# Kernel tuning notes

Hardware: AMD Instinct MI355X
Metric: run time of the kernel (lower is better)

Reference implementation:

```python
import jax, jax.numpy as jnp
import numpy as np

NEUMANN_TERMS = 6  # matches neumann_terms=6 in init_kwargs


def cayley_apply(W, x, terms):
    """Apply Cayley-parameterized unitary U = (I - A)^{-1}(I + A), A = skew(W),
    with the inverse approximated by a truncated Neumann series:
    (I - A)^{-1} z ~= sum_{k=0}^{terms-1} A^k z.  x: [N, d] row vectors."""
    A = 0.5 * (W - W.T)            # skew-symmetric [d, d]
    z = x + x @ A.T                # (I + A) x
    acc = z
    s = z
    for _ in range(terms - 1):     # small fixed loop over Neumann terms
        s = s @ A.T                # A^k z
        acc = acc + s
    return acc


def quantum_activation(h, theta):
    """Parametric quantum rotation: rotate each adjacent feature pair by theta.
    Norm-preserving (unitary) nonlinearity in place of ReLU/GELU."""
    a = h[..., 0::2]
    b = h[..., 1::2]
    c = jnp.cos(theta)
    s = jnp.sin(theta)
    ra = a * c - b * s
    rb = a * s + b * c
    return jnp.stack([ra, rb], axis=-1).reshape(h.shape)


def setup_inputs() -> dict:
    key = jax.random.key(0)
    k1, k2, k3 = jax.random.split(key, 3)
    num_tokens, d_model = 16384, 2048
    x = jax.random.normal(k1, (num_tokens, d_model), dtype=jnp.float32)
    # Orthogonal(gain=0.1)-like init: small-norm weights keep the Neumann series convergent
    u1 = 0.1 * jax.random.normal(k2, (d_model, d_model), dtype=jnp.float32) / jnp.sqrt(d_model)
    u1 = u1 * jnp.sqrt(d_model) * 0.0 + 0.1 * jax.random.orthogonal(k2, d_model, dtype=jnp.float32)
    u2 = 0.1 * jax.random.orthogonal(k3, d_model, dtype=jnp.float32)
    theta = jnp.asarray(0.7854, dtype=jnp.float32)  # pi/4 initializer
    return {"x": x, "u1": u1, "u2": u2, "theta": theta}


def reference(x, u1, u2, theta):
    h = cayley_apply(u1, x, NEUMANN_TERMS)
    h = quantum_activation(h, theta)
    out = cayley_apply(u2, h, NEUMANN_TERMS)
    return out
```

## Files before the change

### kernel.cpp

```cpp
#include <hip/hip_runtime.h>
#include <hip/hip_bf16.h>

#define ND 2048

using bf16 = __hip_bfloat16;
using short8 = __attribute__((ext_vector_type(8))) short;
using floatx4 = __attribute__((ext_vector_type(4))) float;

__device__ __forceinline__ void gl2lds16(const short* g, short* l) {
    __builtin_amdgcn_global_load_lds(
        (const __attribute__((address_space(1))) unsigned int*)g,
        (__attribute__((address_space(3))) unsigned int*)l,
        16, 0, 0);
}


__global__ void build_skew(const float* __restrict__ u, bf16* __restrict__ M) {
    __shared__ float t[32][33];
    const int bx = blockIdx.x & (ND / 32 - 1);
    const int by = blockIdx.x / (ND / 32);
    const int tx = threadIdx.x & 31;
    const int ty = threadIdx.x >> 5;
#pragma unroll
    for (int rr = 0; rr < 4; ++rr) {
        const int r = ty * 4 + rr;
        t[tx][r] = u[(size_t)(bx * 32 + r) * ND + by * 32 + tx];
    }
    __syncthreads();
#pragma unroll
    for (int rr = 0; rr < 4; ++rr) {
        const int r = ty * 4 + rr;
        const size_t idx = (size_t)(by * 32 + r) * ND + bx * 32 + tx;
        M[idx] = __float2bfloat16(0.5f * (t[r][tx] - u[idx]));
    }
}

__global__ void build_hoff1(const bf16* __restrict__ M, const bf16* Msq, bf16* Hoff) {
    const size_t idx = (size_t)blockIdx.x * 256 + threadIdx.x;
    const float m = __bfloat162float(M[idx]);
    const float q = __bfloat162float(Msq[idx]);
    Hoff[idx] = __float2bfloat16(2.f * m + q);
}

__global__ void build_hoff(const bf16* M, const bf16* Msq, bf16* Hoff, bf16* HoffT) {
    const size_t idx = (size_t)blockIdx.x * 256 + threadIdx.x;
    const float m = __bfloat162float(M[idx]);
    const float q = __bfloat162float(Msq[idx]);
    Hoff[idx] = __float2bfloat16(2.f * m + q);
    HoffT[idx] = __float2bfloat16(q - 2.f * m);
}

__global__ void convert_f32_bf16(const float* __restrict__ x, bf16* __restrict__ y) {
    const size_t base = ((size_t)blockIdx.x * 256 + threadIdx.x) * 8;
    const float4 f0 = *(const float4*)(x + base);
    const float4 f1 = *(const float4*)(x + base + 4);
    short8 pk;
    pk[0] = __builtin_bit_cast(short, __float2bfloat16(f0.x));
    pk[1] = __builtin_bit_cast(short, __float2bfloat16(f0.y));
    pk[2] = __builtin_bit_cast(short, __float2bfloat16(f0.z));
    pk[3] = __builtin_bit_cast(short, __float2bfloat16(f0.w));
    pk[4] = __builtin_bit_cast(short, __float2bfloat16(f1.x));
    pk[5] = __builtin_bit_cast(short, __float2bfloat16(f1.y));
    pk[6] = __builtin_bit_cast(short, __float2bfloat16(f1.z));
    pk[7] = __builtin_bit_cast(short, __float2bfloat16(f1.w));
    *(short8*)((short*)y + base) = pk;
}

enum { EPI_PLAIN = 0, EPI_NEG = 1, EPI_ADD1 = 2, EPI_P = 3, EPI_P_ROT = 4, EPI_PT = 5 };

template <int EPI, bool OF32>
__device__ __forceinline__ void gemm_core(
    short* aT, short* bT,
    const bf16* __restrict__ A, const bf16* __restrict__ Bt, void* __restrict__ Cp,
    const int Nc, const int K, const int bx, const int by,
    const bf16* __restrict__ add1, const bf16* __restrict__ add2,
    const float* __restrict__ thetaP)
{
    const int tid = threadIdx.x;
    const int lane = tid & 63;
    const int quad = lane >> 4;
    const int l15 = lane & 15;
    const int wv = tid >> 6;
    const int wr = (wv >> 1) << 6;
    const int wc = (wv & 1) << 6;

    const short* Ag = (const short*)A + (size_t)(by << 7) * K;
    const short* Bg = (const short*)Bt + (size_t)(bx << 7) * K;

    floatx4 acc[4][4];
#pragma unroll
    for (int i = 0; i < 4; ++i)
#pragma unroll
        for (int j = 0; j < 4; ++j)
            acc[i][j] = (floatx4){0.f, 0.f, 0.f, 0.f};

    for (int k0 = 0; k0 < K; k0 += 32) {
#pragma unroll
        for (int c = 0; c < 2; ++c) {
            const int ch = (c << 8) + (wv << 6) + lane;
            const int row = ch >> 2;
            const int kp = (ch & 3) << 3;
            const int ldsBase = ((c << 8) + (wv << 6)) << 3;
            gl2lds16(Ag + (size_t)row * K + k0 + kp, aT + ldsBase);
            gl2lds16(Bg + (size_t)row * K + k0 + kp, bT + ldsBase);
        }
        __syncthreads();
        short8 af[4], bfr[4];
#pragma unroll
        for (int mi = 0; mi < 4; ++mi)
            af[mi] = *(const short8*)(aT + ((wr + (mi << 4) + l15) << 5) + (quad << 3));
#pragma unroll
        for (int ni = 0; ni < 4; ++ni)
            bfr[ni] = *(const short8*)(bT + ((wc + (ni << 4) + l15) << 5) + (quad << 3));
#pragma unroll
        for (int mi = 0; mi < 4; ++mi)
#pragma unroll
            for (int ni = 0; ni < 4; ++ni)
                acc[mi][ni] = __builtin_amdgcn_mfma_f32_16x16x32_bf16(af[mi], bfr[ni], acc[mi][ni], 0, 0, 0);
        __syncthreads();
    }

    float ct = 0.f, st = 0.f;
    if (EPI == EPI_P_ROT) {
        const float th = *thetaP;
        ct = cosf(th);
        st = sinf(th);
    }

#pragma unroll
    for (int mi = 0; mi < 4; ++mi) {
#pragma unroll
        for (int ni = 0; ni < 4; ++ni) {
#pragma unroll
            for (int r = 0; r < 4; ++r) {
                const int row = (by << 7) + wr + (mi << 4) + (quad << 2) + r;
                const int col = (bx << 7) + wc + (ni << 4) + l15;
                const size_t idx = (size_t)row * Nc + col;
                float v = acc[mi][ni][r];
                if (EPI == EPI_NEG) v = -v;
                if (EPI == EPI_ADD1) v += __bfloat162float(add1[idx]);
                if (EPI == EPI_P)
                    v += (row == col ? 1.f : 0.f)
                       + __bfloat162float(add1[idx]) + __bfloat162float(add2[idx]);
                if (EPI == EPI_PT)
                    v += (row == col ? 1.f : 0.f)
                       + __bfloat162float(add1[idx])
                       + __bfloat162float(add2[(size_t)col * Nc + row]);
                if (EPI == EPI_P_ROT) {
                    v += (row == col ? 1.f : 0.f)
                       + __bfloat162float(add1[idx]) + __bfloat162float(add2[idx]);
                    const float w = __shfl_xor(v, 1, 64);
                    v = (l15 & 1) ? (st * w + ct * v) : (ct * v - st * w);
                }
                if (OF32) ((float*)Cp)[idx] = v;
                else      ((bf16*)Cp)[idx] = __float2bfloat16(v);
            }
        }
    }
}

template <int EPI, bool OF32>
__launch_bounds__(256, 2) __global__
void gemm_one(const bf16* __restrict__ A, const bf16* __restrict__ Bt,
              void* __restrict__ Cp, const int Nc, const int K,
              const bf16* __restrict__ add1, const bf16* __restrict__ add2,
              const float* __restrict__ thetaP)
{
    __shared__ __attribute__((aligned(16))) short aT[128 * 32];
    __shared__ __attribute__((aligned(16))) short bT[128 * 32];
    const int nblk = Nc >> 7;
    gemm_core<EPI, OF32>(aT, bT, A, Bt, Cp, Nc, K, blockIdx.x % nblk, blockIdx.x / nblk,
                         add1, add2, thetaP);
}

template <int EPI0, int EPI1>
__launch_bounds__(256, 2) __global__
void gemm_dual(const bf16* A0, const bf16* B0, bf16* C0, const bf16* a10, const bf16* a20,
               const bf16* A1, const bf16* B1, bf16* C1, const bf16* a11, const bf16* a21,
               const float* thetaP)
{
    __shared__ __attribute__((aligned(16))) short aT[128 * 32];
    __shared__ __attribute__((aligned(16))) short bT[128 * 32];
    const int nblk = ND >> 7;
    const int nsub = nblk * nblk;
    int b = blockIdx.x;
    if (b < nsub) {
        gemm_core<EPI0, false>(aT, bT, A0, B0, (void*)C0, ND, ND, b % nblk, b / nblk, a10, a20, thetaP);
    } else {
        b -= nsub;
        gemm_core<EPI1, false>(aT, bT, A1, B1, (void*)C1, ND, ND, b % nblk, b / nblk, a11, a21, thetaP);
    }
}


__device__ __forceinline__ void stage512(short* ldsT, const short* gT, const int K,
                                         const int kb, const int c0,
                                         const int wv, const int lane) {
    const int ch = c0 + (wv << 6) + lane;
    const int rw = ch >> 3;
    const int cs = (ch & 7) ^ (rw & 7);
    gl2lds16(gT + (size_t)rw * K + kb + (cs << 3),
             ldsT + ((c0 + (wv << 6)) << 3));
}

__device__ __forceinline__ void phase_mid() {
    __builtin_amdgcn_sched_barrier(0);
    __builtin_amdgcn_s_barrier();
    asm volatile("s_waitcnt lgkmcnt(0)" ::: "memory");
    __builtin_amdgcn_sched_barrier(0);
    __builtin_amdgcn_s_setprio(1);
}
__device__ __forceinline__ void phase_end() {
    __builtin_amdgcn_s_setprio(0);
    __builtin_amdgcn_sched_barrier(0);
    __builtin_amdgcn_s_barrier();
}

__device__ __forceinline__ void tile256(
    short* Ac, short* Bc, short* An,
    const short* Ag, const short* Bg, const int K, const int nt, const int t,
    const int wv, const int lane, const int aBase, const int bBase,
    const int cOff0, const int cOff1, floatx4 (&acc)[8][4])
{
    short8 af[4][2], bb[4][2];
    const int kb1 = (t + 1) << 6;
    const int kb2 = (t + 2) << 6;

#pragma unroll
    for (int ml = 0; ml < 4; ++ml) {
        af[ml][0] = *(const short8*)(Ac + aBase + (ml << 10) + cOff0);
        af[ml][1] = *(const short8*)(Ac + aBase + (ml << 10) + cOff1);
    }
#pragma unroll
    for (int ni = 0; ni < 2; ++ni) {
        bb[ni][0] = *(const short8*)(Bc + bBase + (ni << 10) + cOff0);
        bb[ni][1] = *(const short8*)(Bc + bBase + (ni << 10) + cOff1);
    }
    if (t + 1 < nt) { stage512(An, Ag, K, kb1, 512, wv, lane); stage512(An, Ag, K, kb1, 1536, wv, lane); }
    phase_mid();
#pragma unroll
    for (int ml = 0; ml < 4; ++ml)
#pragma unroll
        for (int ni = 0; ni < 2; ++ni) {
            acc[ml][ni] = __builtin_amdgcn_mfma_f32_16x16x32_bf16(af[ml][0], bb[ni][0], acc[ml][ni], 0, 0, 0);
            acc[ml][ni] = __builtin_amdgcn_mfma_f32_16x16x32_bf16(af[ml][1], bb[ni][1], acc[ml][ni], 0, 0, 0);
        }
    phase_end();

#pragma unroll
    for (int ni = 2; ni < 4; ++ni) {
        bb[ni][0] = *(const short8*)(Bc + bBase + (ni << 10) + cOff0);
        bb[ni][1] = *(const short8*)(Bc + bBase + (ni << 10) + cOff1);
    }
    if (t + 2 < nt) { stage512(Ac, Ag, K, kb2, 0, wv, lane); stage512(Ac, Ag, K, kb2, 1024, wv, lane); }
    phase_mid();
#pragma unroll
    for (int ml = 0; ml < 4; ++ml)
#pragma unroll
        for (int ni = 2; ni < 4; ++ni) {
            acc[ml][ni] = __builtin_amdgcn_mfma_f32_16x16x32_bf16(af[ml][0], bb[ni][0], acc[ml][ni], 0, 0, 0);
            acc[ml][ni] = __builtin_amdgcn_mfma_f32_16x16x32_bf16(af[ml][1], bb[ni][1], acc[ml][ni], 0, 0, 0);
        }
    phase_end();

#pragma unroll
    for (int ml = 0; ml < 4; ++ml) {
        af[ml][0] = *(const short8*)(Ac + aBase + 4096 + (ml << 10) + cOff0);
        af[ml][1] = *(const short8*)(Ac + aBase + 4096 + (ml << 10) + cOff1);
    }
    if (t + 2 < nt) { stage512(Bc, Bg, K, kb2, 0, wv, lane); stage512(Bc, Bg, K, kb2, 512, wv, lane); }
    phase_mid();
#pragma unroll
    for (int ml = 0; ml < 4; ++ml)
#pragma unroll
        for (int ni = 0; ni < 2; ++ni) {
            acc[4 + ml][ni] = __builtin_amdgcn_mfma_f32_16x16x32_bf16(af[ml][0], bb[ni][0], acc[4 + ml][ni], 0, 0, 0);
            acc[4 + ml][ni] = __builtin_amdgcn_mfma_f32_16x16x32_bf16(af[ml][1], bb[ni][1], acc[4 + ml][ni], 0, 0, 0);
        }
    phase_end();

    if (t + 2 < nt) { stage512(Bc, Bg, K, kb2, 1024, wv, lane); stage512(Bc, Bg, K, kb2, 1536, wv, lane); }
    __builtin_amdgcn_sched_barrier(0);
    if (t < nt - 2) asm volatile("s_waitcnt vmcnt(6)" ::: "memory");
    else            asm volatile("s_waitcnt vmcnt(0)" ::: "memory");
    __builtin_amdgcn_s_barrier();
    __builtin_amdgcn_sched_barrier(0);
    __builtin_amdgcn_s_setprio(1);
#pragma unroll
    for (int ml = 0; ml < 4; ++ml)
#pragma unroll
        for (int ni = 2; ni < 4; ++ni) {
            acc[4 + ml][ni] = __builtin_amdgcn_mfma_f32_16x16x32_bf16(af[ml][0], bb[ni][0], acc[4 + ml][ni], 0, 0, 0);
            acc[4 + ml][ni] = __builtin_amdgcn_mfma_f32_16x16x32_bf16(af[ml][1], bb[ni][1], acc[4 + ml][ni], 0, 0, 0);
        }
    phase_end();
}

__launch_bounds__(512, 2) __global__
void gemm_big256(const bf16* __restrict__ A, const bf16* __restrict__ Bt,
                 float* __restrict__ C, const int Nc, const int K)
{
    __shared__ __attribute__((aligned(16))) short smem[65536];
    short* A0s = smem;
    short* A1s = smem + 16384;
    short* B0s = smem + 32768;
    short* B1s = smem + 49152;

    const int nblkx = Nc >> 8;
    const int bx = blockIdx.x % nblkx;
    const int by = blockIdx.x / nblkx;
    const int tid = threadIdx.x;
    const int lane = tid & 63;
    const int q = lane >> 4;
    const int l15 = lane & 15;
    const int wv = tid >> 6;
    const int wm = wv >> 2;
    const int wn = wv & 3;

    const short* Ag = (const short*)A + (size_t)(by << 8) * K;
    const short* Bg = (const short*)Bt + (size_t)(bx << 8) * K;

    const int swz = l15 & 7;
    const int aBase = ((wm << 7) + l15) << 6;
    const int bBase = ((wn << 6) + l15) << 6;
    const int cOff0 = (q ^ swz) << 3;
    const int cOff1 = ((q + 4) ^ swz) << 3;

    floatx4 acc[8][4];
#pragma unroll
    for (int i = 0; i < 8; ++i)
#pragma unroll
        for (int j = 0; j < 4; ++j)
            acc[i][j] = (floatx4){0.f, 0.f, 0.f, 0.f};

    const int nt = K >> 6;

    stage512(A0s, Ag, K, 0, 0,    wv, lane);
    stage512(A0s, Ag, K, 0, 512,  wv, lane);
    stage512(A0s, Ag, K, 0, 1024, wv, lane);
    stage512(A0s, Ag, K, 0, 1536, wv, lane);
    stage512(B0s, Bg, K, 0, 0,    wv, lane);
    stage512(B0s, Bg, K, 0, 512,  wv, lane);
    stage512(B0s, Bg, K, 0, 1024, wv, lane);
    stage512(B0s, Bg, K, 0, 1536, wv, lane);
    stage512(A1s, Ag, K, 64, 0,    wv, lane);
    stage512(A1s, Ag, K, 64, 1024, wv, lane);
    stage512(B1s, Bg, K, 64, 0,    wv, lane);
    stage512(B1s, Bg, K, 64, 512,  wv, lane);
    stage512(B1s, Bg, K, 64, 1024, wv, lane);
    stage512(B1s, Bg, K, 64, 1536, wv, lane);
    __builtin_amdgcn_sched_barrier(0);
    asm volatile("s_waitcnt vmcnt(6)" ::: "memory");
    __builtin_amdgcn_s_barrier();

    for (int t = 0; t < nt; t += 2) {
        tile256(A0s, B0s, A1s, Ag, Bg, K, nt, t,     wv, lane, aBase, bBase, cOff0, cOff1, acc);
        tile256(A1s, B1s, A0s, Ag, Bg, K, nt, t + 1, wv, lane, aBase, bBase, cOff0, cOff1, acc);
    }

#pragma unroll
    for (int mi = 0; mi < 8; ++mi)
#pragma unroll
        for (int ni = 0; ni < 4; ++ni)
#pragma unroll
            for (int r = 0; r < 4; ++r) {
                const int row = (by << 8) + (wm << 7) + (mi << 4) + (q << 2) + r;
                const int col = (bx << 8) + (wn << 6) + (ni << 4) + l15;
                C[(size_t)row * Nc + col] = acc[mi][ni][r];
            }
}

template <int EPI, bool AF32, bool OF32>
__launch_bounds__(256, 2) __global__
void gemm_bt(const void* __restrict__ Ap, const bf16* __restrict__ Bt,
             void* __restrict__ Cp, const int Nc, const int K,
             const bf16* __restrict__ add1, const bf16* __restrict__ add2,
             const float* __restrict__ thetaP)
{
    __shared__ __attribute__((aligned(16))) short aT[128 * 32];
    __shared__ __attribute__((aligned(16))) short bT[128 * 32];

    const int nblk = Nc >> 7;
    const int bx = blockIdx.x % nblk;
    const int by = blockIdx.x / nblk;
    const int tid = threadIdx.x;
    const int lane = tid & 63;
    const int quad = lane >> 4;
    const int l15 = lane & 15;
    const int wv = tid >> 6;
    const int wr = (wv >> 1) << 6;
    const int wc = (wv & 1) << 6;

    const short* Ag = (const short*)Ap + (size_t)(by << 7) * K;
    const float* Agf = (const float*)Ap + (size_t)(by << 7) * K;
    const short* Bg = (const short*)Bt + (size_t)(bx << 7) * K;

    floatx4 acc[4][4];
#pragma unroll
    for (int i = 0; i < 4; ++i)
#pragma unroll
        for (int j = 0; j < 4; ++j)
            acc[i][j] = (floatx4){0.f, 0.f, 0.f, 0.f};

    for (int k0 = 0; k0 < K; k0 += 32) {
#pragma unroll
        for (int c = 0; c < 2; ++c) {
            const int ch = tid + (c << 8);
            const int row = ch >> 2;
            const int kp = (ch & 3) << 3;
            if (AF32) {
                const float4 f0 = *(const float4*)(Agf + (size_t)row * K + k0 + kp);
                const float4 f1 = *(const float4*)(Agf + (size_t)row * K + k0 + kp + 4);
                short8 pk;
                pk[0] = __builtin_bit_cast(short, __float2bfloat16(f0.x));
                pk[1] = __builtin_bit_cast(short, __float2bfloat16(f0.y));
                pk[2] = __builtin_bit_cast(short, __float2bfloat16(f0.z));
                pk[3] = __builtin_bit_cast(short, __float2bfloat16(f0.w));
                pk[4] = __builtin_bit_cast(short, __float2bfloat16(f1.x));
                pk[5] = __builtin_bit_cast(short, __float2bfloat16(f1.y));
                pk[6] = __builtin_bit_cast(short, __float2bfloat16(f1.z));
                pk[7] = __builtin_bit_cast(short, __float2bfloat16(f1.w));
                *(short8*)(aT + (row << 5) + kp) = pk;
            } else {
                *(int4*)(aT + (row << 5) + kp) = *(const int4*)(Ag + (size_t)row * K + k0 + kp);
            }
            *(int4*)(bT + (row << 5) + kp) = *(const int4*)(Bg + (size_t)row * K + k0 + kp);
        }
        __syncthreads();
        short8 af[4], bfr[4];
#pragma unroll
        for (int mi = 0; mi < 4; ++mi)
            af[mi] = *(const short8*)(aT + ((wr + (mi << 4) + l15) << 5) + (quad << 3));
#pragma unroll
        for (int ni = 0; ni < 4; ++ni)
            bfr[ni] = *(const short8*)(bT + ((wc + (ni << 4) + l15) << 5) + (quad << 3));
#pragma unroll
        for (int mi = 0; mi < 4; ++mi)
#pragma unroll
            for (int ni = 0; ni < 4; ++ni)
                acc[mi][ni] = __builtin_amdgcn_mfma_f32_16x16x32_bf16(af[mi], bfr[ni], acc[mi][ni], 0, 0, 0);
        __syncthreads();
    }

    float ct = 0.f, st = 0.f;
    if (EPI == EPI_P_ROT) {
        const float th = *thetaP;
        ct = cosf(th);
        st = sinf(th);
    }

#pragma unroll
    for (int mi = 0; mi < 4; ++mi) {
#pragma unroll
        for (int ni = 0; ni < 4; ++ni) {
#pragma unroll
            for (int r = 0; r < 4; ++r) {
                const int row = (by << 7) + wr + (mi << 4) + (quad << 2) + r;
                const int col = (bx << 7) + wc + (ni << 4) + l15;
                const size_t idx = (size_t)row * Nc + col;
                float v = acc[mi][ni][r];
                if (EPI == EPI_NEG) v = -v;
                if (EPI == EPI_ADD1) v += __bfloat162float(add1[idx]);
                if (EPI == EPI_P || EPI == EPI_P_ROT)
                    v += (row == col ? 1.f : 0.f)
                       + __bfloat162float(add1[idx]) + __bfloat162float(add2[idx]);
                if (EPI == EPI_P_ROT) {
                    const float w = __shfl_xor(v, 1, 64);
                    v = (l15 & 1) ? (st * w + ct * v) : (ct * v - st * w);
                }
                if (OF32) ((float*)Cp)[idx] = v;
                else      ((bf16*)Cp)[idx] = __float2bfloat16(v);
            }
        }
    }
}


extern "C" void kernel_launch(void* const* d_in, const int* in_sizes, int n_in,
                              void* d_out, int out_size, void* d_ws, size_t ws_size,
                              hipStream_t stream)
{
    const float* x = (const float*)d_in[0];
    const float* u1 = (const float*)d_in[1];
    const float* u2 = (const float*)d_in[2];
    const float* th = (const float*)d_in[3];
    float* out = (float*)d_out;
    const int tokens = in_sizes[0] / ND;

    const size_t MAT = (size_t)ND * ND;
    const size_t XBE = (size_t)tokens * ND;

    const dim3 blk(256);
    const int gSkew = (ND / 32) * (ND / 32);
    const int gElem = (int)(MAT / 256);
    const int gSm = (ND / 128) * (ND / 128);
    const int gBig = (tokens / 128) * (ND / 128);

    if (ws_size >= (6 * MAT + XBE) * sizeof(bf16)) {
        bf16* base = (bf16*)d_ws;
        bf16* b0 = base;
        bf16* b1 = base + MAT;
        bf16* b2 = base + 2 * MAT;
        bf16* b3 = base + 3 * MAT;
        bf16* b4 = base + 4 * MAT;
        bf16* b5 = base + 5 * MAT;
        bf16* xb = base + 6 * MAT;

        convert_f32_bf16<<<(int)(XBE / 2048), blk, 0, stream>>>(x, xb);
        build_skew<<<gSkew, blk, 0, stream>>>(u2, b0);
        build_skew<<<gSkew, blk, 0, stream>>>(u1, b1);
        gemm_dual<EPI_NEG, EPI_NEG><<<2 * gSm, blk, 0, stream>>>(
            b0, b0, b2, nullptr, nullptr,  b1, b1, b3, nullptr, nullptr, nullptr);
        gemm_dual<EPI_ADD1, EPI_ADD1><<<2 * gSm, blk, 0, stream>>>(
            b2, b2, b4, b2, nullptr,  b3, b3, b5, b3, nullptr, nullptr);
        build_hoff1<<<gElem, blk, 0, stream>>>(b0, b2, b2);
        build_hoff1<<<gElem, blk, 0, stream>>>(b1, b3, b3);
        gemm_dual<EPI_PT, EPI_P_ROT><<<2 * gSm, blk, 0, stream>>>(
            b4, b2, b0, b4, b2,  b3, b5, b1, b5, b3, th);
        gemm_one<EPI_PLAIN, false><<<gSm, blk, 0, stream>>>(b0, b1, b2, ND, ND, nullptr, nullptr, nullptr);
        if ((tokens & 255) == 0) {
            const int gBig256 = (tokens >> 8) * (ND >> 8);
            gemm_big256<<<gBig256, dim3(512), 0, stream>>>(xb, b2, out, ND, ND);
        } else {
            gemm_one<EPI_PLAIN, true><<<gBig, blk, 0, stream>>>(xb, b2, out, ND, ND, nullptr, nullptr, nullptr);
        }
    } else {
        bf16* A = (bf16*)d_ws;
        bf16* B = A + MAT;
        bf16* Cb = B + MAT;
        bf16* D = Cb + MAT;
        bf16* E = D + MAT;

        build_skew<<<gSkew, blk, 0, stream>>>(u2, A);
        gemm_bt<EPI_NEG, false, false><<<gSm, blk, 0, stream>>>(A, A, B, ND, ND, nullptr, nullptr, nullptr);
        gemm_bt<EPI_ADD1, false, false><<<gSm, blk, 0, stream>>>(B, B, Cb, ND, ND, B, nullptr, nullptr);
        build_hoff<<<gElem, blk, 0, stream>>>(A, B, D, E);
        gemm_bt<EPI_P, false, false><<<gSm, blk, 0, stream>>>(Cb, D, A, ND, ND, Cb, E, nullptr);

        build_skew<<<gSkew, blk, 0, stream>>>(u1, B);
        gemm_bt<EPI_NEG, false, false><<<gSm, blk, 0, stream>>>(B, B, Cb, ND, ND, nullptr, nullptr, nullptr);
        gemm_bt<EPI_ADD1, false, false><<<gSm, blk, 0, stream>>>(Cb, Cb, D, ND, ND, Cb, nullptr, nullptr);
        build_hoff<<<gElem, blk, 0, stream>>>(B, Cb, E, B);
        gemm_bt<EPI_P_ROT, false, false><<<gSm, blk, 0, stream>>>(E, D, Cb, ND, ND, D, E, th);

        gemm_bt<EPI_PLAIN, false, false><<<gSm, blk, 0, stream>>>(A, Cb, D, ND, ND, nullptr, nullptr, nullptr);
        gemm_bt<EPI_PLAIN, true, true><<<gBig, blk, 0, stream>>>(x, D, out, ND, ND, nullptr, nullptr, nullptr);
    }
}
```

Before: 598.6 us.

## Software-pipeline LDS fragment loads across phases and add XCD-aware block swizzle

Restructures the 256x256 GEMM main loop so that A/B register fragments for the next phase and next k-tile are read from LDS one phase ahead, with partial lgkmcnt waits instead of full drains. The aim is to overlap LDS reads with MFMA work instead of stalling on them. It also remaps block indices so consecutive tiles land on the same XCD, improving L2 reuse across all GEMM kernels. This raises register pressure and depends on hand-tuned vmcnt/lgkmcnt counts, which are easy to get wrong.

```diff
diff --git a/kernel.cpp b/kernel.cpp
--- a/kernel.cpp
+++ b/kernel.cpp
@@ -12,6 +12,11 @@
         (const __attribute__((address_space(1))) unsigned int*)g,
         (__attribute__((address_space(3))) unsigned int*)l,
         16, 0, 0);
+}
+
+__device__ __forceinline__ int xcd_swz(int b, int g) {
+    if ((g & 7) == 0) b = (b & 7) * (g >> 3) + (b >> 3);
+    return b;
 }
 
 
@@ -169,7 +174,8 @@
     __shared__ __attribute__((aligned(16))) short aT[128 * 32];
     __shared__ __attribute__((aligned(16))) short bT[128 * 32];
     const int nblk = Nc >> 7;
-    gemm_core<EPI, OF32>(aT, bT, A, Bt, Cp, Nc, K, blockIdx.x % nblk, blockIdx.x / nblk,
+    const int b = xcd_swz(blockIdx.x, gridDim.x);
+    gemm_core<EPI, OF32>(aT, bT, A, Bt, Cp, Nc, K, b % nblk, b / nblk,
                          add1, add2, thetaP);
 }
 
@@ -183,7 +189,7 @@
     __shared__ __attribute__((aligned(16))) short bT[128 * 32];
     const int nblk = ND >> 7;
     const int nsub = nblk * nblk;
-    int b = blockIdx.x;
+    int b = xcd_swz(blockIdx.x, gridDim.x);
     if (b < nsub) {
         gemm_core<EPI0, false>(aT, bT, A0, B0, (void*)C0, ND, ND, b % nblk, b / nblk, a10, a20, thetaP);
     } else {
@@ -203,86 +209,104 @@
              ldsT + ((c0 + (wv << 6)) << 3));
 }
 
-__device__ __forceinline__ void phase_mid() {
-    __builtin_amdgcn_sched_barrier(0);
-    __builtin_amdgcn_s_barrier();
-    asm volatile("s_waitcnt lgkmcnt(0)" ::: "memory");
-    __builtin_amdgcn_sched_barrier(0);
-    __builtin_amdgcn_s_setprio(1);
-}
 __device__ __forceinline__ void phase_end() {
     __builtin_amdgcn_s_setprio(0);
     __builtin_amdgcn_sched_barrier(0);
     __builtin_amdgcn_s_barrier();
 }
 
-__device__ __forceinline__ void tile256(
-    short* Ac, short* Bc, short* An,
+#define MFMA_BF16 __builtin_amdgcn_mfma_f32_16x16x32_bf16
+
+__device__ __forceinline__ void tile256p(
+    short* Ac, short* Bc, short* An, short* Bn,
     const short* Ag, const short* Bg, const int K, const int nt, const int t,
     const int wv, const int lane, const int aBase, const int bBase,
-    const int cOff0, const int cOff1, floatx4 (&acc)[8][4])
-{
-    short8 af[4][2], bb[4][2];
+    const int cOff0, const int cOff1,
+    short8 (&afLo)[4][2], short8 (&afHi)[4][2], short8 (&bb)[4][2],
+    floatx4 (&acc)[8][4])
+{
     const int kb1 = (t + 1) << 6;
     const int kb2 = (t + 2) << 6;
-
-#pragma unroll
-    for (int ml = 0; ml < 4; ++ml) {
-        af[ml][0] = *(const short8*)(Ac + aBase + (ml << 10) + cOff0);
-        af[ml][1] = *(const short8*)(Ac + aBase + (ml << 10) + cOff1);
-    }
-#pragma unroll
-    for (int ni = 0; ni < 2; ++ni) {
-        bb[ni][0] = *(const short8*)(Bc + bBase + (ni << 10) + cOff0);
-        bb[ni][1] = *(const short8*)(Bc + bBase + (ni << 10) + cOff1);
-    }
-    if (t + 1 < nt) { stage512(An, Ag, K, kb1, 512, wv, lane); stage512(An, Ag, K, kb1, 1536, wv, lane); }
-    phase_mid();
-#pragma unroll
-    for (int ml = 0; ml < 4; ++ml)
-#pragma unroll
-        for (int ni = 0; ni < 2; ++ni) {
-            acc[ml][ni] = __builtin_amdgcn_mfma_f32_16x16x32_bf16(af[ml][0], bb[ni][0], acc[ml][ni], 0, 0, 0);
-            acc[ml][ni] = __builtin_amdgcn_mfma_f32_16x16x32_bf16(af[ml][1], bb[ni][1], acc[ml][ni], 0, 0, 0);
-        }
-    phase_end();
+    const bool sfull = (t < nt - 2);
 
 #pragma unroll
     for (int ni = 2; ni < 4; ++ni) {
         bb[ni][0] = *(const short8*)(Bc + bBase + (ni << 10) + cOff0);
         bb[ni][1] = *(const short8*)(Bc + bBase + (ni << 10) + cOff1);
     }
+#pragma unroll
+    for (int ml = 0; ml < 4; ++ml) {
+        afHi[ml][0] = *(const short8*)(Ac + aBase + 4096 + (ml << 10) + cOff0);
+        afHi[ml][1] = *(const short8*)(Ac + aBase + 4096 + (ml << 10) + cOff1);
+    }
+    if (t + 1 < nt) { stage512(An, Ag, K, kb1, 512, wv, lane); stage512(An, Ag, K, kb1, 1536, wv, lane); }
+    __builtin_amdgcn_sched_barrier(0);
+    __builtin_amdgcn_s_barrier();
+    asm volatile("s_waitcnt lgkmcnt(12)" ::: "memory");
+    __builtin_amdgcn_sched_barrier(0);
+    __builtin_amdgcn_s_setprio(1);
+#pragma unroll
+    for (int ml = 0; ml < 4; ++ml)
+#pragma unroll
+        for (int ni = 0; ni < 2; ++ni) {
+            acc[ml][ni] = MFMA_BF16(afLo[ml][0], bb[ni][0], acc[ml][ni], 0, 0, 0);
+            acc[ml][ni] = MFMA_BF16(afLo[ml][1], bb[ni][1], acc[ml][ni], 0, 0, 0);
+        }
+    phase_end();
+
     if (t + 2 < nt) { stage512(Ac, Ag, K, kb2, 0, wv, lane); stage512(Ac, Ag, K, kb2, 1024, wv, lane); }
-    phase_mid();
+    __builtin_amdgcn_sched_barrier(0);
+    if (sfull) asm volatile("s_waitcnt vmcnt(8)" ::: "memory");
+    else       asm volatile("s_waitcnt vmcnt(0)" ::: "memory");
+    __builtin_amdgcn_s_barrier();
+    asm volatile("s_waitcnt lgkmcnt(8)" ::: "memory");
+    __builtin_amdgcn_sched_barrier(0);
+    __builtin_amdgcn_s_setprio(1);
 #pragma unroll
     for (int ml = 0; ml < 4; ++ml)
 #pragma unroll
         for (int ni = 2; ni < 4; ++ni) {
-            acc[ml][ni] = __builtin_amdgcn_mfma_f32_16x16x32_bf16(af[ml][0], bb[ni][0], acc[ml][ni], 0, 0, 0);
-            acc[ml][ni] = __builtin_amdgcn_mfma_f32_16x16x32_bf16(af[ml][1], bb[ni][1], acc[ml][ni], 0, 0, 0);
+            acc[ml][ni] = MFMA_BF16(afLo[ml][0], bb[ni][0], acc[ml][ni], 0, 0, 0);
+            acc[ml][ni] = MFMA_BF16(afLo[ml][1], bb[ni][1], acc[ml][ni], 0, 0, 0);
         }
     phase_end();
 
-#pragma unroll
-    for (int ml = 0; ml < 4; ++ml) {
-        af[ml][0] = *(const short8*)(Ac + aBase + 4096 + (ml << 10) + cOff0);
-        af[ml][1] = *(const short8*)(Ac + aBase + 4096 + (ml << 10) + cOff1);
+    if (t + 1 < nt) {
+#pragma unroll
+        for (int ml = 0; ml < 4; ++ml) {
+            afLo[ml][0] = *(const short8*)(An + aBase + (ml << 10) + cOff0);
+            afLo[ml][1] = *(const short8*)(An + aBase + (ml << 10) + cOff1);
+        }
     }
     if (t + 2 < nt) { stage512(Bc, Bg, K, kb2, 0, wv, lane); stage512(Bc, Bg, K, kb2, 512, wv, lane); }
-    phase_mid();
+    __builtin_amdgcn_sched_barrier(0);
+    if (sfull) asm volatile("s_waitcnt vmcnt(6)" ::: "memory");
+    else       asm volatile("s_waitcnt vmcnt(0)" ::: "memory");
+    __builtin_amdgcn_s_barrier();
+    if (t + 1 < nt) asm volatile("s_waitcnt lgkmcnt(8)" ::: "memory");
+    else            asm volatile("s_waitcnt lgkmcnt(0)" ::: "memory");
+    __builtin_amdgcn_sched_barrier(0);
+    __builtin_amdgcn_s_setprio(1);
 #pragma unroll
     for (int ml = 0; ml < 4; ++ml)
 #pragma unroll
         for (int ni = 0; ni < 2; ++ni) {
-            acc[4 + ml][ni] = __builtin_amdgcn_mfma_f32_16x16x32_bf16(af[ml][0], bb[ni][0], acc[4 + ml][ni], 0, 0, 0);
-            acc[4 + ml][ni] = __builtin_amdgcn_mfma_f32_16x16x32_bf16(af[ml][1], bb[ni][1], acc[4 + ml][ni], 0, 0, 0);
+            acc[4 + ml][ni] = MFMA_BF16(afHi[ml][0], bb[ni][0], acc[4 + ml][ni], 0, 0, 0);
+            acc[4 + ml][ni] = MFMA_BF16(afHi[ml][1], bb[ni][1], acc[4 + ml][ni], 0, 0, 0);
         }
     phase_end();
 
+    if (t + 1 < nt) {
+#pragma unroll
+        for (int ni = 0; ni < 2; ++ni) {
+            bb[ni][0] = *(const short8*)(Bn + bBase + (ni << 10) + cOff0);
+            bb[ni][1] = *(const short8*)(Bn + bBase + (ni << 10) + cOff1);
+        }
+    }
     if (t + 2 < nt) { stage512(Bc, Bg, K, kb2, 1024, wv, lane); stage512(Bc, Bg, K, kb2, 1536, wv, lane); }
     __builtin_amdgcn_sched_barrier(0);
-    if (t < nt - 2) asm volatile("s_waitcnt vmcnt(6)" ::: "memory");
-    else            asm volatile("s_waitcnt vmcnt(0)" ::: "memory");
+    if (sfull) asm volatile("s_waitcnt vmcnt(6)" ::: "memory");
+    else       asm volatile("s_waitcnt vmcnt(0)" ::: "memory");
     __builtin_amdgcn_s_barrier();
     __builtin_amdgcn_sched_barrier(0);
     __builtin_amdgcn_s_setprio(1);
@@ -290,8 +314,8 @@
     for (int ml = 0; ml < 4; ++ml)
 #pragma unroll
         for (int ni = 2; ni < 4; ++ni) {
-            acc[4 + ml][ni] = __builtin_amdgcn_mfma_f32_16x16x32_bf16(af[ml][0], bb[ni][0], acc[4 + ml][ni], 0, 0, 0);
-            acc[4 + ml][ni] = __builtin_amdgcn_mfma_f32_16x16x32_bf16(af[ml][1], bb[ni][1], acc[4 + ml][ni], 0, 0, 0);
+            acc[4 + ml][ni] = MFMA_BF16(afHi[ml][0], bb[ni][0], acc[4 + ml][ni], 0, 0, 0);
+            acc[4 + ml][ni] = MFMA_BF16(afHi[ml][1], bb[ni][1], acc[4 + ml][ni], 0, 0, 0);
         }
     phase_end();
 }
@@ -307,8 +331,9 @@
     short* B1s = smem + 49152;
 
     const int nblkx = Nc >> 8;
-    const int bx = blockIdx.x % nblkx;
-    const int by = blockIdx.x / nblkx;
+    const int b = xcd_swz(blockIdx.x, gridDim.x);
+    const int bx = b % nblkx;
+    const int by = b / nblkx;
     const int tid = threadIdx.x;
     const int lane = tid & 63;
     const int q = lane >> 4;
@@ -332,6 +357,8 @@
 #pragma unroll
         for (int j = 0; j < 4; ++j)
             acc[i][j] = (floatx4){0.f, 0.f, 0.f, 0.f};
+
+    short8 afLo[4][2], afHi[4][2], bb[4][2];
 
     const int nt = K >> 6;
 
@@ -352,10 +379,24 @@
     __builtin_amdgcn_sched_barrier(0);
     asm volatile("s_waitcnt vmcnt(6)" ::: "memory");
     __builtin_amdgcn_s_barrier();
+    __builtin_amdgcn_sched_barrier(0);
+#pragma unroll
+    for (int ml = 0; ml < 4; ++ml) {
+        afLo[ml][0] = *(const short8*)(A0s + aBase + (ml << 10) + cOff0);
+        afLo[ml][1] = *(const short8*)(A0s + aBase + (ml << 10) + cOff1);
+    }
+#pragma unroll
+    for (int ni = 0; ni < 2; ++ni) {
+        bb[ni][0] = *(const short8*)(B0s + bBase + (ni << 10) + cOff0);
+        bb[ni][1] = *(const short8*)(B0s + bBase + (ni << 10) + cOff1);
+    }
+    __builtin_amdgcn_sched_barrier(0);
 
     for (int t = 0; t < nt; t += 2) {
-        tile256(A0s, B0s, A1s, Ag, Bg, K, nt, t,     wv, lane, aBase, bBase, cOff0, cOff1, acc);
-        tile256(A1s, B1s, A0s, Ag, Bg, K, nt, t + 1, wv, lane, aBase, bBase, cOff0, cOff1, acc);
+        tile256p(A0s, B0s, A1s, B1s, Ag, Bg, K, nt, t,
+                 wv, lane, aBase, bBase, cOff0, cOff1, afLo, afHi, bb, acc);
+        tile256p(A1s, B1s, A0s, B0s, Ag, Bg, K, nt, t + 1,
+                 wv, lane, aBase, bBase, cOff0, cOff1, afLo, afHi, bb, acc);
     }
 
 #pragma unroll
```

Result: faster. 584.3 us (-2.4%).
